# Performance work log

Measured on AMD Instinct MI355X. Metric: run time of the kernel, lower is better.

## Reference

```python
import jax, jax.numpy as jnp
import numpy as np

B, S, HID = 2, 2048, 4096
NH, NKV, HD = 32, 8, 128
MAX_POS = 4096
SCALE = HD ** -0.5


def _rope_tables():
    inv_freq = 1.0 / (10000.0 ** (np.arange(0, HD, 2, dtype=np.float32) / HD))
    t = np.arange(MAX_POS, dtype=np.float32)
    freqs = np.outer(t, inv_freq)              # [MAX_POS, HD/2]
    emb = np.concatenate([freqs, freqs], axis=-1)  # [MAX_POS, HD]
    return jnp.asarray(np.cos(emb)), jnp.asarray(np.sin(emb))


def setup_inputs() -> dict:
    key = jax.random.key(0)
    ks = jax.random.split(key, 6)
    hidden_states = jax.random.normal(ks[0], (B, S, HID), dtype=jnp.float32)
    position_ids = jnp.broadcast_to(jnp.arange(S, dtype=jnp.int64 if jax.config.jax_enable_x64 else jnp.int32), (B, S))
    cos_table, sin_table = _rope_tables()
    # weights stored [in, out] for x @ W
    sd = HID ** -0.5
    Wq = jax.random.normal(ks[1], (HID, NH * HD), dtype=jnp.float32) * sd
    Wk = jax.random.normal(ks[2], (HID, NKV * HD), dtype=jnp.float32) * sd
    Wv = jax.random.normal(ks[3], (HID, NKV * HD), dtype=jnp.float32) * sd
    Wo = jax.random.normal(ks[4], (NH * HD, HID), dtype=jnp.float32) * sd
    return {"hidden_states": hidden_states, "position_ids": position_ids,
            "cos_table": cos_table, "sin_table": sin_table,
            "Wq": Wq, "Wk": Wk, "Wv": Wv, "Wo": Wo}


def _rotate_half(x):
    x1, x2 = jnp.split(x, 2, axis=-1)
    return jnp.concatenate([-x2, x1], axis=-1)


def reference(hidden_states, position_ids, cos_table, sin_table, Wq, Wk, Wv, Wo):
    b, s, _ = hidden_states.shape
    q = (hidden_states @ Wq).reshape(b, s, NH, HD)
    k = (hidden_states @ Wk).reshape(b, s, NKV, HD)
    v = (hidden_states @ Wv).reshape(b, s, NKV, HD)

    # RoPE, cos/sin gathered by position and unsqueezed at head dim (dim=2, bsnd)
    cos = cos_table[position_ids][:, :, None, :]  # [b, s, 1, hd]
    sin = sin_table[position_ids][:, :, None, :]
    q = q * cos + _rotate_half(q) * sin
    k = k * cos + _rotate_half(k) * sin

    # GQA: expand kv heads to match query heads
    rep = NH // NKV
    k = jnp.repeat(k, rep, axis=2)  # [b, s, NH, hd]
    v = jnp.repeat(v, rep, axis=2)

    scores = jnp.einsum('bqnd,bknd->bnqk', q, k) * SCALE  # [b, NH, s, s]
    causal = jnp.tril(jnp.ones((s, s), dtype=bool))
    scores = jnp.where(causal, scores, jnp.finfo(scores.dtype).min)
    probs = jax.nn.softmax(scores, axis=-1)
    attn = jnp.einsum('bnqk,bknd->bqnd', probs, v)  # [b, s, NH, hd]
    attn = attn.reshape(b, s, NH * HD)
    return attn @ Wo
```

## Files before the change

### kernel.cpp

```cpp
#include <hip/hip_runtime.h>
#include <stdint.h>

typedef unsigned short u16;
typedef __bf16 bf16x8 __attribute__((ext_vector_type(8)));
typedef unsigned short u16x8 __attribute__((ext_vector_type(8)));
typedef unsigned short u16x4 __attribute__((ext_vector_type(4)));
typedef float f32x4 __attribute__((ext_vector_type(4)));

#define B_ 2
#define S_ 2048
#define HID_ 4096
#define NH_ 32
#define NKV_ 8
#define HD_ 128
#define NTOT_ 6144
#define SCALE_ 0.08838834764831845f

#define GLD16(gp, lp)                                                     \
  __builtin_amdgcn_global_load_lds(                                       \
      (__attribute__((address_space(1))) void*)(gp),                      \
      (__attribute__((address_space(3))) void*)(lp), 16, 0, 0)

__device__ __forceinline__ u16 f2b(float f) {
  union { float f; uint32_t u; } v; v.f = f;
  uint32_t u = v.u;
  u = u + 0x7fffu + ((u >> 16) & 1u);
  return (u16)(u >> 16);
}
__device__ __forceinline__ float b2f(u16 s) {
  union { uint32_t u; float f; } v; v.u = ((uint32_t)s) << 16;
  return v.f;
}
__device__ __forceinline__ bf16x8 ldb8(const u16* p) {
  u16x8 u = *(const u16x8*)p;
  return __builtin_bit_cast(bf16x8, u);
}
__device__ __forceinline__ bf16x8 ldb8b(const char* p) {
  u16x8 u = *(const u16x8*)p;
  return __builtin_bit_cast(bf16x8, u);
}

__global__ __launch_bounds__(256) void k_convx(const float* __restrict__ src,
                                               u16* __restrict__ dst, int n4) {
  int i = blockIdx.x * 256 + threadIdx.x;
  if (i >= n4) return;
  const float4 v = ((const float4*)src)[i];
  u16x4 o = { f2b(v.x), f2b(v.y), f2b(v.z), f2b(v.w) };
  *(u16x4*)(dst + (size_t)i * 4) = o;
}

__global__ __launch_bounds__(256) void k_convT(const float* __restrict__ src,
                                               u16* __restrict__ dst, int N, int Kd) {
  __shared__ u16 tile[64][65];
  int k0 = blockIdx.x * 64, n0 = blockIdx.y * 64;
  int t = threadIdx.x;
  int rr = t >> 4;
  int cc = (t & 15) * 4;
#pragma unroll
  for (int p = 0; p < 4; ++p) {
    int r = p * 16 + rr;
    float4 v = *(const float4*)&src[(size_t)(k0 + r) * N + n0 + cc];
    tile[cc + 0][r] = f2b(v.x);
    tile[cc + 1][r] = f2b(v.y);
    tile[cc + 2][r] = f2b(v.z);
    tile[cc + 3][r] = f2b(v.w);
  }
  __syncthreads();
#pragma unroll
  for (int p = 0; p < 4; ++p) {
    int n = p * 16 + rr;
    u16x4 o = { tile[n][cc], tile[n][cc + 1], tile[n][cc + 2], tile[n][cc + 3] };
    *(u16x4*)&dst[(size_t)(n0 + n) * Kd + k0 + cc] = o;
  }
}

template <int MODE>
__global__ __launch_bounds__(256) void k_gemm(const u16* __restrict__ A,
                                              const u16* __restrict__ Bt,
                                              float* __restrict__ Cf,
                                              u16* __restrict__ Qb,
                                              u16* __restrict__ Kb,
                                              u16* __restrict__ Vb,
                                              int M, int N, int Kd) {
  __shared__ __align__(16) u16 As[128][32];
  __shared__ __align__(16) u16 Bs[128][32];
  int m0 = blockIdx.y * 128, n0 = blockIdx.x * 128;
  int t = threadIdx.x, lane = t & 63, wave = t >> 6;
  int wr = wave >> 1, wc = wave & 1;
  int lg = lane >> 4, l16 = lane & 15;
  f32x4 acc[4][4] = {};

  const u16* Ap = A  + (size_t)(m0 + wave * 32 + (lane >> 2)) * Kd + (lane & 3) * 8;
  const u16* Bp = Bt + (size_t)(n0 + wave * 32 + (lane >> 2)) * Kd + (lane & 3) * 8;
  u16* AsW = &As[wave * 32][0];
  u16* BsW = &Bs[wave * 32][0];

  for (int k0 = 0; k0 < Kd; k0 += 32) {
    __syncthreads();
    GLD16(Ap,           AsW);
    GLD16(Ap + 16 * Kd, AsW + 16 * 32);
    GLD16(Bp,           BsW);
    GLD16(Bp + 16 * Kd, BsW + 16 * 32);
    Ap += 32; Bp += 32;
    __syncthreads();
    bf16x8 af[4], bfr[4];
#pragma unroll
    for (int i = 0; i < 4; ++i) {
      af[i]  = ldb8(&As[wr * 64 + i * 16 + l16][lg * 8]);
      bfr[i] = ldb8(&Bs[wc * 64 + i * 16 + l16][lg * 8]);
    }
#pragma unroll
    for (int i = 0; i < 4; ++i)
#pragma unroll
      for (int j = 0; j < 4; ++j)
        acc[i][j] = __builtin_amdgcn_mfma_f32_16x16x32_bf16(af[i], bfr[j], acc[i][j], 0, 0, 0);
  }

  if (MODE == 1) {
#pragma unroll
    for (int i = 0; i < 4; ++i)
#pragma unroll
      for (int j = 0; j < 4; ++j)
#pragma unroll
        for (int r = 0; r < 4; ++r) {
          int m = m0 + wr * 64 + i * 16 + lg * 4 + r;
          int n = n0 + wc * 64 + j * 16 + l16;
          Cf[(size_t)m * N + n] = acc[i][j][r];
        }
  } else {
    int head = n0 >> 7;
#pragma unroll
    for (int i = 0; i < 4; ++i)
#pragma unroll
      for (int j = 0; j < 4; ++j)
#pragma unroll
        for (int r = 0; r < 4; ++r) {
          int m = m0 + wr * 64 + i * 16 + lg * 4 + r;
          int d = wc * 64 + j * 16 + l16;
          int b = m >> 11, s = m & (S_ - 1);
          u16 val = f2b(acc[i][j][r]);
          if (head < NH_) {
            Qb[(((size_t)b * NH_ + head) * S_ + s) * HD_ + d] = val;
          } else if (head < NH_ + NKV_) {
            Kb[(((size_t)b * NKV_ + (head - NH_)) * S_ + s) * HD_ + d] = val;
          } else {
            Vb[(((size_t)b * NKV_ + (head - NH_ - NKV_)) * HD_ + d) * S_ + s] = val;
          }
        }
  }
}

__global__ __launch_bounds__(256) void k_rope(u16* __restrict__ buf, const int* __restrict__ pos,
                                              const float* __restrict__ ct, const float* __restrict__ st,
                                              int H, int rows) {
  int wave = threadIdx.x >> 6, lane = threadIdx.x & 63;
  int row = blockIdx.x * 4 + wave;
  if (row >= rows) return;
  int s = row & (S_ - 1);
  int b = row / (H * S_);
  int p = pos[b * S_ + s];
  size_t base = (size_t)row * HD_;
  float x1 = b2f(buf[base + lane]);
  float x2 = b2f(buf[base + 64 + lane]);
  float c  = ct[(size_t)p * HD_ + lane];
  float sn = st[(size_t)p * HD_ + lane];
  buf[base + lane]      = f2b(x1 * c - x2 * sn);
  buf[base + 64 + lane] = f2b(x2 * c + x1 * sn);
}

__global__ __launch_bounds__(256, 4) void k_attn(const u16* __restrict__ Q,
                                                 const u16* __restrict__ K,
                                                 const u16* __restrict__ Vt,
                                                 u16* __restrict__ Ob) {
  __shared__ __align__(16) char smem[40960];
  const int VS_OFF = 16384, PS_OFF = 32768;

  int bid = blockIdx.x;
  int pid = bid & 15;
  int h   = (bid >> 4) & 31;
  int b   = bid >> 9;
  int kvh = h >> 2;
  int tid = threadIdx.x;
  int wave = tid >> 6, lane = tid & 63;
  int lg = lane >> 4, l16 = lane & 15;
  int lsw = (l16 & 7) << 4;

  const u16* Qp = Q  + (((size_t)b * NH_  + h)   * S_) * HD_;
  const u16* Kp = K  + (((size_t)b * NKV_ + kvh) * S_) * HD_;
  const u16* Vp = Vt + (((size_t)b * NKV_ + kvh) * HD_) * S_;

  for (int pass = 0; pass < 2; ++pass) {
    int qt = pass ? (31 - pid) : pid;
    int q0 = qt * 64 + wave * 16;
    int qg = q0 + l16;

    bf16x8 qf[4];
#pragma unroll
    for (int c = 0; c < 4; ++c)
      qf[c] = ldb8(&Qp[(size_t)qg * HD_ + c * 32 + lg * 8]);

    f32x4 oacc[8] = {};
    float mrun = -1e30f, lrun = 0.f;

    int nt = qt + 1;
    for (int tI = 0; tI < nt; ++tI) {
      int kb = tI * 64;
      __syncthreads();
#pragma unroll
      for (int i = 0; i < 4; ++i) {
        int ci = i * 256 + tid;
        int r = ci >> 4, ch = ci & 15;
        u16x8 v = *(const u16x8*)&Kp[(size_t)(kb + r) * HD_ + ch * 8];
        *(u16x8*)(smem + r * 256 + ((ch * 16) ^ ((r & 7) << 4))) = v;
      }
#pragma unroll
      for (int i = 0; i < 4; ++i) {
        int ci = i * 256 + tid;
        int r = ci >> 3, ch = ci & 7;
        u16x8 v = *(const u16x8*)&Vp[(size_t)r * S_ + kb + ch * 8];
        *(u16x8*)(smem + VS_OFF + r * 128 + ((ch * 16) ^ ((r & 7) << 4))) = v;
      }
      __syncthreads();

      f32x4 sc[4] = {};
#pragma unroll
      for (int c = 0; c < 4; ++c) {
#pragma unroll
        for (int n = 0; n < 4; ++n) {
          bf16x8 kf = ldb8b(smem + (n * 16 + l16) * 256 + ((c * 64 + lg * 16) ^ lsw));
          sc[n] = __builtin_amdgcn_mfma_f32_16x16x32_bf16(kf, qf[c], sc[n], 0, 0, 0);
        }
      }

      bool diag = (tI == qt);
      float mx = -1e30f;
#pragma unroll
      for (int n = 0; n < 4; ++n)
#pragma unroll
        for (int r = 0; r < 4; ++r) {
          float v = sc[n][r];
          int key = kb + n * 16 + lg * 4 + r;
          if (diag && key > qg) v = -1e30f;
          sc[n][r] = v;
          mx = fmaxf(mx, v);
        }
      mx = fmaxf(mx, __shfl_xor(mx, 16));
      mx = fmaxf(mx, __shfl_xor(mx, 32));
      float mnew = fmaxf(mrun, mx * SCALE_);
      float alpha = __expf(mrun - mnew);
      float ps = 0.f;
#pragma unroll
      for (int n = 0; n < 4; ++n) {
        u16x4 pk;
#pragma unroll
        for (int r = 0; r < 4; ++r) {
          float p = __expf(fmaf(sc[n][r], SCALE_, -mnew));
          ps += p;
          pk[r] = f2b(p);
        }
        *(u16x4*)(smem + PS_OFF + wave * 2048 + l16 * 128 + ((n * 32 + lg * 8) ^ lsw)) = pk;
      }
      ps += __shfl_xor(ps, 16);
      ps += __shfl_xor(ps, 32);
      lrun = lrun * alpha + ps;
      mrun = mnew;

      float ar[4];
#pragma unroll
      for (int r = 0; r < 4; ++r) ar[r] = __shfl(alpha, lg * 4 + r);
#pragma unroll
      for (int ns = 0; ns < 8; ++ns)
#pragma unroll
        for (int r = 0; r < 4; ++r) oacc[ns][r] *= ar[r];

#pragma unroll
      for (int ck = 0; ck < 2; ++ck) {
        bf16x8 pa = ldb8b(smem + PS_OFF + wave * 2048 + l16 * 128 + ((ck * 64 + lg * 16) ^ lsw));
#pragma unroll
        for (int ns = 0; ns < 8; ++ns) {
          bf16x8 vf = ldb8b(smem + VS_OFF + (ns * 16 + l16) * 128 + ((ck * 64 + lg * 16) ^ lsw));
          oacc[ns] = __builtin_amdgcn_mfma_f32_16x16x32_bf16(pa, vf, oacc[ns], 0, 0, 0);
        }
      }
    }

    float lr[4];
#pragma unroll
    for (int r = 0; r < 4; ++r) lr[r] = 1.0f / __shfl(lrun, lg * 4 + r);
#pragma unroll
    for (int ns = 0; ns < 8; ++ns)
#pragma unroll
      for (int r = 0; r < 4; ++r) {
        int q = q0 + lg * 4 + r;
        Ob[((size_t)(b * S_) + q) * (NH_ * HD_) + h * HD_ + ns * 16 + l16] =
            f2b(oacc[ns][r] * lr[r]);
      }
  }
}

extern "C" void kernel_launch(void* const* d_in, const int* in_sizes, int n_in,
                              void* d_out, int out_size, void* d_ws, size_t ws_size,
                              hipStream_t stream) {
  const float* hs  = (const float*)d_in[0];
  const int*   pos = (const int*)d_in[1];
  const float* ct  = (const float*)d_in[2];
  const float* st  = (const float*)d_in[3];
  const float* Wq  = (const float*)d_in[4];
  const float* Wk  = (const float*)d_in[5];
  const float* Wv  = (const float*)d_in[6];
  const float* Wo  = (const float*)d_in[7];
  float* out = (float*)d_out;

  char* w = (char*)d_ws;
  u16* Xb    = (u16*)(w);
  u16* WqkvT = (u16*)(w + 33554432ull);
  u16* WoT   = (u16*)(w + 83886080ull);
  u16* Qb    = (u16*)(w + 117440512ull);
  u16* Kb    = (u16*)(w + 150994944ull);
  u16* Vb    = (u16*)(w + 159383552ull);
  u16* Attb  = (u16*)(w + 167772160ull);

  k_convx<<<16384, 256, 0, stream>>>(hs, Xb, 4194304);
  k_convT<<<dim3(64, 64), 256, 0, stream>>>(Wq, WqkvT, 4096, 4096);
  k_convT<<<dim3(64, 16), 256, 0, stream>>>(Wk, WqkvT + (size_t)4096 * 4096, 1024, 4096);
  k_convT<<<dim3(64, 16), 256, 0, stream>>>(Wv, WqkvT + (size_t)5120 * 4096, 1024, 4096);
  k_convT<<<dim3(64, 64), 256, 0, stream>>>(Wo, WoT, 4096, 4096);
  k_gemm<0><<<dim3(48, 32), 256, 0, stream>>>(Xb, WqkvT, nullptr, Qb, Kb, Vb, 4096, NTOT_, 4096);
  k_rope<<<32768, 256, 0, stream>>>(Qb, pos, ct, st, NH_, B_ * NH_ * S_);
  k_rope<<<8192, 256, 0, stream>>>(Kb, pos, ct, st, NKV_, B_ * NKV_ * S_);
  k_attn<<<1024, 256, 0, stream>>>(Qb, Kb, Vb, Attb);
  k_gemm<1><<<dim3(32, 32), 256, 0, stream>>>(Attb, WoT, out, nullptr, nullptr, nullptr, 4096, 4096, 4096);
}
```

Before: 715.4 us.

## Rewrite GEMM with 256x256 tiles, 4-stage LDS pipeline, swizzled LDS and XCD-aware block mapping

Rewrites the bf16 GEMM to use 256x256 block tiles with 512 threads and a four-deep ring of LDS buffers filled by async global-to-LDS loads, so loads are issued three k-steps ahead. It adds an XOR swizzle on LDS chunks to avoid bank conflicts, s_setprio around the MFMA bursts, and a block-index remap that groups tiles per XCD for L2 reuse. The intent is to raise arithmetic intensity and hide global memory latency in both projection GEMMs. In exchange it uses 128 KB of LDS and many more accumulator registers per thread, and the grid shrinks to 384 and 256 blocks, which risks under-filling the CUs.

Result: faster. 670.0 us (-6.3%).

```diff
diff --git a/kernel.cpp b/kernel.cpp
--- a/kernel.cpp
+++ b/kernel.cpp
@@ -75,76 +75,117 @@
 }
 
 template <int MODE>
-__global__ __launch_bounds__(256) void k_gemm(const u16* __restrict__ A,
-                                              const u16* __restrict__ Bt,
-                                              float* __restrict__ Cf,
-                                              u16* __restrict__ Qb,
-                                              u16* __restrict__ Kb,
-                                              u16* __restrict__ Vb,
-                                              int M, int N, int Kd) {
-  __shared__ __align__(16) u16 As[128][32];
-  __shared__ __align__(16) u16 Bs[128][32];
-  int m0 = blockIdx.y * 128, n0 = blockIdx.x * 128;
+__global__ __launch_bounds__(512, 2) void k_gemm(const u16* __restrict__ A,
+                                                 const u16* __restrict__ Bt,
+                                                 float* __restrict__ Cf,
+                                                 u16* __restrict__ Qb,
+                                                 u16* __restrict__ Kb,
+                                                 u16* __restrict__ Vb,
+                                                 int M, int N, int Kd) {
+  __shared__ __align__(16) char smem[131072];
+  const int NT = Kd >> 5;
+
+  int nwg = gridDim.x * gridDim.y;
+  int orig = blockIdx.y * gridDim.x + blockIdx.x;
+  int cpx = nwg >> 3;
+  int swz = (orig & 7) * cpx + (orig >> 3);
+  int bx = swz % gridDim.x, by = swz / gridDim.x;
+  int m0 = by * 256, n0 = bx * 256;
+
   int t = threadIdx.x, lane = t & 63, wave = t >> 6;
-  int wr = wave >> 1, wc = wave & 1;
+  int wr = wave >> 2, wc = wave & 3;
   int lg = lane >> 4, l16 = lane & 15;
-  f32x4 acc[4][4] = {};
-
-  const u16* Ap = A  + (size_t)(m0 + wave * 32 + (lane >> 2)) * Kd + (lane & 3) * 8;
-  const u16* Bp = Bt + (size_t)(n0 + wave * 32 + (lane >> 2)) * Kd + (lane & 3) * 8;
-  u16* AsW = &As[wave * 32][0];
-  u16* BsW = &Bs[wave * 32][0];
-
-  for (int k0 = 0; k0 < Kd; k0 += 32) {
-    __syncthreads();
-    GLD16(Ap,           AsW);
-    GLD16(Ap + 16 * Kd, AsW + 16 * 32);
-    GLD16(Bp,           BsW);
-    GLD16(Bp + 16 * Kd, BsW + 16 * 32);
-    Ap += 32; Bp += 32;
-    __syncthreads();
-    bf16x8 af[4], bfr[4];
-#pragma unroll
-    for (int i = 0; i < 4; ++i) {
-      af[i]  = ldb8(&As[wr * 64 + i * 16 + l16][lg * 8]);
-      bfr[i] = ldb8(&Bs[wc * 64 + i * 16 + l16][lg * 8]);
-    }
+  int loff = l16 * 64 + ((lg ^ ((l16 >> 1) & 3)) << 4);
+
+  int srow = lane >> 2;
+  int schk = (lane & 3) ^ ((lane >> 3) & 3);
+  const u16* sA0 = A  + (size_t)(m0 + wave * 16 + srow) * Kd + schk * 8;
+  const u16* sA1 = sA0 + (size_t)128 * Kd;
+  const u16* sB0 = Bt + (size_t)(n0 + wave * 16 + srow) * Kd + schk * 8;
+  const u16* sB1 = sB0 + (size_t)128 * Kd;
+
+  f32x4 acc[8][4] = {};
+
+#define STAGE_A(kt) do { char* dst_ = smem + ((kt) & 3) * 32768 + wave * 1024;          \
+    GLD16(sA0 + (size_t)(kt) * 32, dst_); GLD16(sA1 + (size_t)(kt) * 32, dst_ + 8192); } while (0)
+#define STAGE_B(kt) do { char* dst_ = smem + ((kt) & 3) * 32768 + 16384 + wave * 1024;  \
+    GLD16(sB0 + (size_t)(kt) * 32, dst_); GLD16(sB1 + (size_t)(kt) * 32, dst_ + 8192); } while (0)
+
+  STAGE_A(0); STAGE_B(0);
+  STAGE_A(1); STAGE_B(1);
+  STAGE_A(2); STAGE_B(2);
+  asm volatile("s_waitcnt vmcnt(8)" ::: "memory");
+  __syncthreads();
+
+  for (int kt = 0; kt < NT; ++kt) {
+    char* Ab = smem + (kt & 3) * 32768;
+    char* Bb = Ab + 16384;
+    bf16x8 bfr[4], af[4];
+#pragma unroll
+    for (int j = 0; j < 4; ++j) bfr[j] = ldb8b(Bb + (wc * 4 + j) * 1024 + loff);
+#pragma unroll
+    for (int i = 0; i < 4; ++i) af[i] = ldb8b(Ab + (wr * 8 + i) * 1024 + loff);
+    if (kt + 3 < NT) STAGE_A(kt + 3);
+    __builtin_amdgcn_s_setprio(1);
 #pragma unroll
     for (int i = 0; i < 4; ++i)
 #pragma unroll
       for (int j = 0; j < 4; ++j)
         acc[i][j] = __builtin_amdgcn_mfma_f32_16x16x32_bf16(af[i], bfr[j], acc[i][j], 0, 0, 0);
-  }
+    __builtin_amdgcn_s_setprio(0);
+#pragma unroll
+    for (int i = 0; i < 4; ++i) af[i] = ldb8b(Ab + (wr * 8 + 4 + i) * 1024 + loff);
+    if (kt + 3 < NT) STAGE_B(kt + 3);
+    __builtin_amdgcn_s_setprio(1);
+#pragma unroll
+    for (int i = 0; i < 4; ++i)
+#pragma unroll
+      for (int j = 0; j < 4; ++j)
+        acc[4 + i][j] = __builtin_amdgcn_mfma_f32_16x16x32_bf16(af[i], bfr[j], acc[4 + i][j], 0, 0, 0);
+    __builtin_amdgcn_s_setprio(0);
+    if (kt < NT - 3) {
+      asm volatile("s_waitcnt vmcnt(8)" ::: "memory");
+      __syncthreads();
+    } else if (kt == NT - 3) {
+      asm volatile("s_waitcnt vmcnt(4)" ::: "memory");
+      __syncthreads();
+    } else if (kt == NT - 2) {
+      asm volatile("s_waitcnt vmcnt(0)" ::: "memory");
+      __syncthreads();
+    }
+  }
+#undef STAGE_A
+#undef STAGE_B
 
   if (MODE == 1) {
 #pragma unroll
-    for (int i = 0; i < 4; ++i)
+    for (int i = 0; i < 8; ++i)
 #pragma unroll
       for (int j = 0; j < 4; ++j)
 #pragma unroll
         for (int r = 0; r < 4; ++r) {
-          int m = m0 + wr * 64 + i * 16 + lg * 4 + r;
+          int m = m0 + wr * 128 + i * 16 + lg * 4 + r;
           int n = n0 + wc * 64 + j * 16 + l16;
           Cf[(size_t)m * N + n] = acc[i][j][r];
         }
   } else {
-    int head = n0 >> 7;
-#pragma unroll
-    for (int i = 0; i < 4; ++i)
+    int slice = (n0 >> 7) + (wc >> 1);
+#pragma unroll
+    for (int i = 0; i < 8; ++i)
 #pragma unroll
       for (int j = 0; j < 4; ++j)
 #pragma unroll
         for (int r = 0; r < 4; ++r) {
-          int m = m0 + wr * 64 + i * 16 + lg * 4 + r;
-          int d = wc * 64 + j * 16 + l16;
+          int m = m0 + wr * 128 + i * 16 + lg * 4 + r;
+          int d = ((wc & 1) << 6) + j * 16 + l16;
           int b = m >> 11, s = m & (S_ - 1);
           u16 val = f2b(acc[i][j][r]);
-          if (head < NH_) {
-            Qb[(((size_t)b * NH_ + head) * S_ + s) * HD_ + d] = val;
-          } else if (head < NH_ + NKV_) {
-            Kb[(((size_t)b * NKV_ + (head - NH_)) * S_ + s) * HD_ + d] = val;
+          if (slice < NH_) {
+            Qb[(((size_t)b * NH_ + slice) * S_ + s) * HD_ + d] = val;
+          } else if (slice < NH_ + NKV_) {
+            Kb[(((size_t)b * NKV_ + (slice - NH_)) * S_ + s) * HD_ + d] = val;
           } else {
-            Vb[(((size_t)b * NKV_ + (head - NH_ - NKV_)) * HD_ + d) * S_ + s] = val;
+            Vb[(((size_t)b * NKV_ + (slice - NH_ - NKV_)) * HD_ + d) * S_ + s] = val;
           }
         }
   }
@@ -325,9 +366,9 @@
   k_convT<<<dim3(64, 16), 256, 0, stream>>>(Wk, WqkvT + (size_t)4096 * 4096, 1024, 4096);
   k_convT<<<dim3(64, 16), 256, 0, stream>>>(Wv, WqkvT + (size_t)5120 * 4096, 1024, 4096);
   k_convT<<<dim3(64, 64), 256, 0, stream>>>(Wo, WoT, 4096, 4096);
-  k_gemm<0><<<dim3(48, 32), 256, 0, stream>>>(Xb, WqkvT, nullptr, Qb, Kb, Vb, 4096, NTOT_, 4096);
+  k_gemm<0><<<dim3(24, 16), 512, 0, stream>>>(Xb, WqkvT, nullptr, Qb, Kb, Vb, 4096, NTOT_, 4096);
   k_rope<<<32768, 256, 0, stream>>>(Qb, pos, ct, st, NH_, B_ * NH_ * S_);
   k_rope<<<8192, 256, 0, stream>>>(Kb, pos, ct, st, NKV_, B_ * NKV_ * S_);
   k_attn<<<1024, 256, 0, stream>>>(Qb, Kb, Vb, Attb);
-  k_gemm<1><<<dim3(32, 32), 256, 0, stream>>>(Attb, WoT, out, nullptr, nullptr, nullptr, 4096, 4096, 4096);
-}
+  k_gemm<1><<<dim3(16, 16), 512, 0, stream>>>(Attb, WoT, out, nullptr, nullptr, nullptr, 4096, 4096, 4096);
+}
```

## Replace GEMMs with 256-wide double-buffered, swizzled 8-wave pipelined kernels

Applied to the files above, without the earlier changes.

Both projection GEMMs move from a simple 128x128 single-buffer loop to 512-thread kernels with 256x256 (output) and 256x192 (QKV) tiles. Each kernel double-buffers 64-wide K stages in LDS with an XOR-swizzled layout, interleaves global-to-LDS prefetch with MFMA phases using explicit vmcnt waits, barriers and setprio, and remaps workgroups in a chiplet-aware order. The aim is to hide load latency, avoid LDS bank conflicts and raise arithmetic intensity per tile. In exchange it uses large LDS allocations (up to 128 KB) that limit occupancy to one block per CU, and relies on fragile hand-written wait counts.

Result: faster. 616.0 us (-13.9%).

```diff
diff --git a/kernel.cpp b/kernel.cpp
--- a/kernel.cpp
+++ b/kernel.cpp
@@ -20,6 +20,12 @@
   __builtin_amdgcn_global_load_lds(                                       \
       (__attribute__((address_space(1))) void*)(gp),                      \
       (__attribute__((address_space(3))) void*)(lp), 16, 0, 0)
+
+#define BAR __builtin_amdgcn_s_barrier()
+#define PRIO1 __builtin_amdgcn_s_setprio(1)
+#define PRIO0 __builtin_amdgcn_s_setprio(0)
+#define VM8 asm volatile("s_waitcnt vmcnt(8)" ::: "memory")
+#define VM0 asm volatile("s_waitcnt vmcnt(0)" ::: "memory")
 
 __device__ __forceinline__ u16 f2b(float f) {
   union { float f; uint32_t u; } v; v.f = f;
@@ -74,80 +80,189 @@
   }
 }
 
-template <int MODE>
-__global__ __launch_bounds__(256) void k_gemm(const u16* __restrict__ A,
+__global__ __launch_bounds__(512) void k_gemm_out(const u16* __restrict__ A,
+                                                  const u16* __restrict__ Bt,
+                                                  float* __restrict__ Cf,
+                                                  int M, int N, int Kd) {
+  __shared__ __align__(16) char smem[131072];
+  const int NT = Kd >> 6;
+
+  int nwg = gridDim.x * gridDim.y;
+  int orig = blockIdx.y * gridDim.x + blockIdx.x;
+  int cpx = nwg >> 3;
+  int swz = (orig & 7) * cpx + (orig >> 3);
+  int bx = swz % gridDim.x, by = swz / gridDim.x;
+  int m0 = by * 256, n0 = bx * 256;
+
+  int t = threadIdx.x, lane = t & 63, wave = t >> 6;
+  int wr = wave >> 2, wc = wave & 3;
+  int lg = lane >> 4, l16 = lane & 15;
+  int loff = l16 * 64 + ((lg ^ ((l16 >> 1) & 3)) << 4);
+  int srow = lane >> 2, schk = (lane & 3) ^ ((lane >> 3) & 3);
+
+  const u16* Asrc = A  + (size_t)(m0 + wave * 32 + srow) * Kd + schk * 8;
+  const u16* Bsrc = Bt + (size_t)(n0 + wave * 32 + srow) * Kd + schk * 8;
+
+  f32x4 acc[8][4] = {};
+
+#define OST_A(tile, kc, BB) do {                                              \
+    char* d_ = smem + (BB) + ((kc) << 14) + (wave << 11);                     \
+    const u16* s_ = Asrc + (size_t)(tile) * 64 + (kc) * 32;                   \
+    GLD16(s_, d_); GLD16(s_ + (size_t)16 * Kd, d_ + 1024); } while (0)
+#define OST_B(tile, kc, BB) do {                                              \
+    char* d_ = smem + (BB) + 32768 + ((kc) << 14) + (wave << 11);             \
+    const u16* s_ = Bsrc + (size_t)(tile) * 64 + (kc) * 32;                   \
+    GLD16(s_, d_); GLD16(s_ + (size_t)16 * Kd, d_ + 1024); } while (0)
+#define OLDB(BB, kc) do { _Pragma("unroll")                                   \
+    for (int j = 0; j < 4; ++j)                                               \
+      bfr[j] = ldb8b(smem + (BB) + 32768 + ((kc) << 14) + ((wc * 4 + j) << 10) + loff); } while (0)
+#define OLDA(BB, kc, mh) do { _Pragma("unroll")                               \
+    for (int i = 0; i < 4; ++i)                                               \
+      af[i] = ldb8b(smem + (BB) + ((kc) << 14) + ((wr * 8 + (mh) * 4 + i) << 10) + loff); } while (0)
+#define OMFMA(mh) do { _Pragma("unroll")                                      \
+    for (int i = 0; i < 4; ++i) { _Pragma("unroll")                           \
+      for (int j = 0; j < 4; ++j)                                             \
+        acc[(mh) * 4 + i][j] = __builtin_amdgcn_mfma_f32_16x16x32_bf16(af[i], bfr[j], acc[(mh) * 4 + i][j], 0, 0, 0); } } while (0)
+
+  OST_A(0, 0, 0); OST_B(0, 0, 0); OST_A(0, 1, 0); OST_B(0, 1, 0);
+  OST_A(1, 0, 65536); OST_B(1, 0, 65536);
+  VM8; BAR;
+
+  for (int it = 0; it < (NT >> 1); ++it) {
+    int a = it << 1;
+    bool pf = (a + 2 < NT);
+    bf16x8 bfr[4], af[4];
+    OLDB(0, 0); OLDA(0, 0, 0); OST_A(a + 1, 1, 65536);
+    BAR; PRIO1; OMFMA(0); PRIO0; BAR;
+    OLDA(0, 0, 1); OST_B(a + 1, 1, 65536);
+    BAR; PRIO1; OMFMA(1); PRIO0; if (pf) { VM8; } else { VM0; } BAR;
+    OLDB(0, 1); OLDA(0, 1, 0); if (pf) OST_A(a + 2, 0, 0);
+    BAR; PRIO1; OMFMA(0); PRIO0; BAR;
+    OLDA(0, 1, 1); if (pf) OST_B(a + 2, 0, 0);
+    BAR; PRIO1; OMFMA(1); PRIO0; if (pf) { VM8; } else { VM0; } BAR;
+    OLDB(65536, 0); OLDA(65536, 0, 0); if (pf) OST_A(a + 2, 1, 0);
+    BAR; PRIO1; OMFMA(0); PRIO0; BAR;
+    OLDA(65536, 0, 1); if (pf) OST_B(a + 2, 1, 0);
+    BAR; PRIO1; OMFMA(1); PRIO0; if (pf) { VM8; } else { VM0; } BAR;
+    OLDB(65536, 1); OLDA(65536, 1, 0); if (pf) OST_A(a + 3, 0, 65536);
+    BAR; PRIO1; OMFMA(0); PRIO0; BAR;
+    OLDA(65536, 1, 1); if (pf) OST_B(a + 3, 0, 65536);
+    BAR; PRIO1; OMFMA(1); PRIO0; if (pf) { VM8; } else { VM0; } BAR;
+  }
+#undef OST_A
+#undef OST_B
+#undef OLDB
+#undef OLDA
+#undef OMFMA
+
+#pragma unroll
+  for (int i = 0; i < 8; ++i)
+#pragma unroll
+    for (int j = 0; j < 4; ++j)
+#pragma unroll
+      for (int r = 0; r < 4; ++r) {
+        int m = m0 + wr * 128 + i * 16 + lg * 4 + r;
+        int n = n0 + wc * 64 + j * 16 + l16;
+        Cf[(size_t)m * N + n] = acc[i][j][r];
+      }
+}
+
+__global__ __launch_bounds__(512) void k_gqkv(const u16* __restrict__ A,
                                               const u16* __restrict__ Bt,
-                                              float* __restrict__ Cf,
                                               u16* __restrict__ Qb,
                                               u16* __restrict__ Kb,
-                                              u16* __restrict__ Vb,
-                                              int M, int N, int Kd) {
-  __shared__ __align__(16) u16 As[128][32];
-  __shared__ __align__(16) u16 Bs[128][32];
-  int m0 = blockIdx.y * 128, n0 = blockIdx.x * 128;
+                                              u16* __restrict__ Vb) {
+  __shared__ __align__(16) char smem[114688];
+  const int Kd = HID_;
+  const int NT = Kd >> 6;
+
+  int orig = blockIdx.y * 32 + blockIdx.x;
+  int swz = (orig & 7) * 64 + (orig >> 3);
+  int bx = swz & 31, by = swz >> 5;
+  int m0 = by * 256, n0 = bx * 192;
+
   int t = threadIdx.x, lane = t & 63, wave = t >> 6;
-  int wr = wave >> 1, wc = wave & 1;
+  int wr = wave >> 2, wc = wave & 3;
   int lg = lane >> 4, l16 = lane & 15;
-  f32x4 acc[4][4] = {};
-
-  const u16* Ap = A  + (size_t)(m0 + wave * 32 + (lane >> 2)) * Kd + (lane & 3) * 8;
-  const u16* Bp = Bt + (size_t)(n0 + wave * 32 + (lane >> 2)) * Kd + (lane & 3) * 8;
-  u16* AsW = &As[wave * 32][0];
-  u16* BsW = &Bs[wave * 32][0];
-
-  for (int k0 = 0; k0 < Kd; k0 += 32) {
-    __syncthreads();
-    GLD16(Ap,           AsW);
-    GLD16(Ap + 16 * Kd, AsW + 16 * 32);
-    GLD16(Bp,           BsW);
-    GLD16(Bp + 16 * Kd, BsW + 16 * 32);
-    Ap += 32; Bp += 32;
-    __syncthreads();
-    bf16x8 af[4], bfr[4];
-#pragma unroll
-    for (int i = 0; i < 4; ++i) {
-      af[i]  = ldb8(&As[wr * 64 + i * 16 + l16][lg * 8]);
-      bfr[i] = ldb8(&Bs[wc * 64 + i * 16 + l16][lg * 8]);
-    }
-#pragma unroll
-    for (int i = 0; i < 4; ++i)
-#pragma unroll
-      for (int j = 0; j < 4; ++j)
-        acc[i][j] = __builtin_amdgcn_mfma_f32_16x16x32_bf16(af[i], bfr[j], acc[i][j], 0, 0, 0);
+  int loff = l16 * 64 + ((lg ^ ((l16 >> 1) & 3)) << 4);
+  int srow = lane >> 2, schk = (lane & 3) ^ ((lane >> 3) & 3);
+
+  const u16* Asrc = A + (size_t)(m0 + wave * 32 + srow) * Kd + schk * 8;
+  const u16* sB0 = Bt + (size_t)(n0 + wave * 16 + srow) * Kd + schk * 8;
+  const u16* sB1 = Bt + (size_t)(n0 + 128 + (wave & 3) * 16 + srow) * Kd + schk * 8;
+  int bdst2 = (8 + (wave & 3)) << 10;
+
+  f32x4 acc[8][3] = {};
+
+#define QST_A(tile, kc, BB) do {                                              \
+    char* d_ = smem + (BB) + ((kc) << 14) + (wave << 11);                     \
+    const u16* s_ = Asrc + (size_t)(tile) * 64 + (kc) * 32;                   \
+    GLD16(s_, d_); GLD16(s_ + (size_t)16 * Kd, d_ + 1024); } while (0)
+#define QST_B(tile, kc, BB) do {                                              \
+    char* db_ = smem + (BB) + 32768 + (kc) * 12288;                           \
+    GLD16(sB0 + (size_t)(tile) * 64 + (kc) * 32, db_ + (wave << 10));         \
+    GLD16(sB1 + (size_t)(tile) * 64 + (kc) * 32, db_ + bdst2); } while (0)
+#define QLDB(BB, kc) do { _Pragma("unroll")                                   \
+    for (int j = 0; j < 3; ++j)                                               \
+      bfr[j] = ldb8b(smem + (BB) + 32768 + (kc) * 12288 + ((wc * 3 + j) << 10) + loff); } while (0)
+#define QLDA(BB, kc, mh) do { _Pragma("unroll")                               \
+    for (int i = 0; i < 4; ++i)                                               \
+      af[i] = ldb8b(smem + (BB) + ((kc) << 14) + ((wr * 8 + (mh) * 4 + i) << 10) + loff); } while (0)
+#define QMFMA(mh) do { _Pragma("unroll")                                      \
+    for (int i = 0; i < 4; ++i) { _Pragma("unroll")                           \
+      for (int j = 0; j < 3; ++j)                                             \
+        acc[(mh) * 4 + i][j] = __builtin_amdgcn_mfma_f32_16x16x32_bf16(af[i], bfr[j], acc[(mh) * 4 + i][j], 0, 0, 0); } } while (0)
+
+  QST_A(0, 0, 0); QST_B(0, 0, 0); QST_A(0, 1, 0); QST_B(0, 1, 0);
+  QST_A(1, 0, 57344); QST_B(1, 0, 57344);
+  VM8; BAR;
+
+  for (int it = 0; it < (NT >> 1); ++it) {
+    int a = it << 1;
+    bool pf = (a + 2 < NT);
+    bf16x8 bfr[3], af[4];
+    QLDB(0, 0); QLDA(0, 0, 0); QST_A(a + 1, 1, 57344);
+    BAR; PRIO1; QMFMA(0); PRIO0; BAR;
+    QLDA(0, 0, 1); QST_B(a + 1, 1, 57344);
+    BAR; PRIO1; QMFMA(1); PRIO0; if (pf) { VM8; } else { VM0; } BAR;
+    QLDB(0, 1); QLDA(0, 1, 0); if (pf) QST_A(a + 2, 0, 0);
+    BAR; PRIO1; QMFMA(0); PRIO0; BAR;
+    QLDA(0, 1, 1); if (pf) QST_B(a + 2, 0, 0);
+    BAR; PRIO1; QMFMA(1); PRIO0; if (pf) { VM8; } else { VM0; } BAR;
+    QLDB(57344, 0); QLDA(57344, 0, 0); if (pf) QST_A(a + 2, 1, 0);
+    BAR; PRIO1; QMFMA(0); PRIO0; BAR;
+    QLDA(57344, 0, 1); if (pf) QST_B(a + 2, 1, 0);
+    BAR; PRIO1; QMFMA(1); PRIO0; if (pf) { VM8; } else { VM0; } BAR;
+    QLDB(57344, 1); QLDA(57344, 1, 0); if (pf) QST_A(a + 3, 0, 57344);
+    BAR; PRIO1; QMFMA(0); PRIO0; BAR;
+    QLDA(57344, 1, 1); if (pf) QST_B(a + 3, 0, 57344);
+    BAR; PRIO1; QMFMA(1); PRIO0; if (pf) { VM8; } else { VM0; } BAR;
   }
-
-  if (MODE == 1) {
-#pragma unroll
-    for (int i = 0; i < 4; ++i)
-#pragma unroll
-      for (int j = 0; j < 4; ++j)
-#pragma unroll
-        for (int r = 0; r < 4; ++r) {
-          int m = m0 + wr * 64 + i * 16 + lg * 4 + r;
-          int n = n0 + wc * 64 + j * 16 + l16;
-          Cf[(size_t)m * N + n] = acc[i][j][r];
+#undef QST_A
+#undef QST_B
+#undef QLDB
+#undef QLDA
+#undef QMFMA
+
+#pragma unroll
+  for (int i = 0; i < 8; ++i)
+#pragma unroll
+    for (int j = 0; j < 3; ++j)
+#pragma unroll
+      for (int r = 0; r < 4; ++r) {
+        int m = m0 + wr * 128 + i * 16 + lg * 4 + r;
+        int n = n0 + wc * 48 + j * 16 + l16;
+        int head = n >> 7, d = n & 127;
+        int b = m >> 11, s = m & (S_ - 1);
+        u16 val = f2b(acc[i][j][r]);
+        if (head < NH_) {
+          Qb[(((size_t)b * NH_ + head) * S_ + s) * HD_ + d] = val;
+        } else if (head < NH_ + NKV_) {
+          Kb[(((size_t)b * NKV_ + (head - NH_)) * S_ + s) * HD_ + d] = val;
+        } else {
+          Vb[(((size_t)b * NKV_ + (head - NH_ - NKV_)) * HD_ + d) * S_ + s] = val;
         }
-  } else {
-    int head = n0 >> 7;
-#pragma unroll
-    for (int i = 0; i < 4; ++i)
-#pragma unroll
-      for (int j = 0; j < 4; ++j)
-#pragma unroll
-        for (int r = 0; r < 4; ++r) {
-          int m = m0 + wr * 64 + i * 16 + lg * 4 + r;
-          int d = wc * 64 + j * 16 + l16;
-          int b = m >> 11, s = m & (S_ - 1);
-          u16 val = f2b(acc[i][j][r]);
-          if (head < NH_) {
-            Qb[(((size_t)b * NH_ + head) * S_ + s) * HD_ + d] = val;
-          } else if (head < NH_ + NKV_) {
-            Kb[(((size_t)b * NKV_ + (head - NH_)) * S_ + s) * HD_ + d] = val;
-          } else {
-            Vb[(((size_t)b * NKV_ + (head - NH_ - NKV_)) * HD_ + d) * S_ + s] = val;
-          }
-        }
-  }
+      }
 }
 
 __global__ __launch_bounds__(256) void k_rope(u16* __restrict__ buf, const int* __restrict__ pos,
@@ -325,9 +440,9 @@
   k_convT<<<dim3(64, 16), 256, 0, stream>>>(Wk, WqkvT + (size_t)4096 * 4096, 1024, 4096);
   k_convT<<<dim3(64, 16), 256, 0, stream>>>(Wv, WqkvT + (size_t)5120 * 4096, 1024, 4096);
   k_convT<<<dim3(64, 64), 256, 0, stream>>>(Wo, WoT, 4096, 4096);
-  k_gemm<0><<<dim3(48, 32), 256, 0, stream>>>(Xb, WqkvT, nullptr, Qb, Kb, Vb, 4096, NTOT_, 4096);
+  k_gqkv<<<dim3(32, 16), 512, 0, stream>>>(Xb, WqkvT, Qb, Kb, Vb);
   k_rope<<<32768, 256, 0, stream>>>(Qb, pos, ct, st, NH_, B_ * NH_ * S_);
   k_rope<<<8192, 256, 0, stream>>>(Kb, pos, ct, st, NKV_, B_ * NKV_ * S_);
   k_attn<<<1024, 256, 0, stream>>>(Qb, Kb, Vb, Attb);
-  k_gemm<1><<<dim3(32, 32), 256, 0, stream>>>(Attb, WoT, out, nullptr, nullptr, nullptr, 4096, 4096, 4096);
-}
+  k_gemm_out<<<dim3(16, 16), 512, 0, stream>>>(Attb, WoT, out, 4096, 4096, 4096);
+}
```
